# Performance work log

Measured on AMD Instinct MI355X. Metric: run time of the kernel, lower is better.

## Reference

```python
import jax, jax.numpy as jnp
import numpy as np

BS, DX, DY = 64, 512, 512


def setup_inputs() -> dict:
    key = jax.random.key(0)
    k1, k2, k3, k4, k5 = jax.random.split(key, 5)
    # ~1/3 of bins are zero -> ragged nonzero counts per sample
    hist = jax.random.randint(k1, (BS, DX, DY), 0, 3).astype(jnp.float32)
    xlo = jax.random.uniform(k2, (BS,)) * -5.0
    ylo = jax.random.uniform(k3, (BS,)) * -5.0
    x_lims = jnp.stack([xlo, xlo + 1.0 + 9.0 * jax.random.uniform(k4, (BS,))], axis=1)
    y_lims = jnp.stack([ylo, ylo + 1.0 + 9.0 * jax.random.uniform(k5, (BS,))], axis=1)
    return {"hist": hist, "x_lims": x_lims, "y_lims": y_lims}


def _grids(hist, x_lims, y_lims):
    bs, dx, dy = hist.shape
    cxw = (x_lims[:, 1] - x_lims[:, 0]) / dx  # [bs]
    cyw = (y_lims[:, 1] - y_lims[:, 0]) / dy
    cx = (jnp.linspace(0.0, 1.0, dx)[None, :] * cxw[:, None] * (dx - 1)
          + x_lims[:, 0:1] + cxw[:, None] / 2.0)  # [bs, dx]
    cy = (jnp.linspace(0.0, 1.0, dy)[None, :] * cyw[:, None] * (dy - 1)
          + y_lims[:, 0:1] + cyw[:, None] / 2.0)  # [bs, dy]
    hc = jnp.clip(hist, 0.0, 1.0)
    grid_x = cx[:, :, None] * hc  # [bs, dx, dy]
    grid_y = cy[:, None, :] * hc
    return grid_x, grid_y


def reference(hist, x_lims, y_lims):
    # as_sequence=True path. Data-dependent pad_sequence length is not
    # jit-able, so we pad to the full grid length L=dx*dy; the first lens[b]
    # entries per row match torch's ragged output, the rest are zeros
    # (torch's pad value). Stream compaction = stable argsort on the mask.
    bs, dx, dy = hist.shape
    L = dx * dy
    grid_x, grid_y = _grids(hist, x_lims, y_lims)
    mask = (hist != 0).reshape(bs, L)
    order = jnp.argsort(jnp.where(mask, 0, 1).astype(jnp.int32), axis=1, stable=True)
    pc_x = jnp.take_along_axis(grid_x.reshape(bs, L), order, axis=1)
    pc_y = jnp.take_along_axis(grid_y.reshape(bs, L), order, axis=1)
    pc_w = jnp.take_along_axis(hist.reshape(bs, L), order, axis=1)
    pc_w = jnp.where(jnp.take_along_axis(mask, order, axis=1), pc_w, 0.0)
    pc_lens = mask.sum(axis=1).astype(jnp.int32)  # [bs]
    return jnp.stack([pc_x, pc_y], axis=-1), pc_w, pc_lens
```

## Files before the change

kernel.cpp:

```cpp
#include <hip/hip_runtime.h>

#define BS 64
#define DX 512
#define DY 512
#define L (DX * DY)
#define TILE 4096
#define T_PER_S (L / TILE)
#define THREADS 256
#define EPT (TILE / THREADS)

typedef float vfloat2 __attribute__((ext_vector_type(2)));
typedef float vfloat4 __attribute__((ext_vector_type(4)));

__global__ __launch_bounds__(THREADS) void htpc_count(
    const float* __restrict__ hist, int* __restrict__ tile_count) {
  const int tile = blockIdx.x;
  const float4* h4 = (const float4*)(hist + (size_t)tile * TILE);

  int cnt = 0;
#pragma unroll
  for (int r = 0; r < EPT / 4; ++r) {
    float4 v = h4[r * THREADS + threadIdx.x];
    cnt += (v.x != 0.f) + (v.y != 0.f) + (v.z != 0.f) + (v.w != 0.f);
  }
  const int lane = threadIdx.x & 63;
  const int wv = threadIdx.x >> 6;
#pragma unroll
  for (int d = 32; d > 0; d >>= 1) cnt += __shfl_down(cnt, d);
  __shared__ int ws[THREADS / 64];
  if (lane == 0) ws[wv] = cnt;
  __syncthreads();
  if (threadIdx.x == 0)
    tile_count[tile] = ws[0] + ws[1] + ws[2] + ws[3];
}

__global__ __launch_bounds__(THREADS) void htpc_fused(
    const float* __restrict__ hist, const float* __restrict__ x_lims,
    const float* __restrict__ y_lims, const int* __restrict__ tile_count,
    float* __restrict__ out_pc, float* __restrict__ out_w,
    float* __restrict__ out_lens) {
  __shared__ int sidx[TILE];
  __shared__ float sw[TILE];
  __shared__ int s_off[T_PER_S + 1];
  __shared__ int wsum[THREADS / 64];

  const int tile = blockIdx.x;
  const int b = tile >> 6;
  const int t = tile & 63;
  const size_t gbase = (size_t)tile * TILE + (size_t)threadIdx.x * EPT;
  const float4* h4 = (const float4*)(hist + gbase);

  float v[EPT];
#pragma unroll
  for (int i = 0; i < EPT / 4; ++i) {
    float4 a = h4[i];
    v[i * 4 + 0] = a.x;
    v[i * 4 + 1] = a.y;
    v[i * 4 + 2] = a.z;
    v[i * 4 + 3] = a.w;
  }

  if (threadIdx.x < 64) {
    const int c = tile_count[b * T_PER_S + threadIdx.x];
    int incl = c;
#pragma unroll
    for (int d = 1; d < 64; d <<= 1) {
      int n = __shfl_up(incl, d);
      if ((int)threadIdx.x >= d) incl += n;
    }
    s_off[threadIdx.x] = incl - c;
    if (threadIdx.x == 63) {
      s_off[T_PER_S] = incl;
      if (t == 0) out_lens[b] = (float)incl;
    }
  }

  int cnt = 0;
#pragma unroll
  for (int i = 0; i < EPT; ++i) cnt += (v[i] != 0.f);

  const int lane = threadIdx.x & 63;
  const int wv = threadIdx.x >> 6;
  int incl = cnt;
#pragma unroll
  for (int d = 1; d < 64; d <<= 1) {
    int n = __shfl_up(incl, d);
    if (lane >= d) incl += n;
  }
  if (lane == 63) wsum[wv] = incl;
  __syncthreads();
  int wbase = 0, total = 0;
#pragma unroll
  for (int i = 0; i < THREADS / 64; ++i) {
    int s = wsum[i];
    if (i < wv) wbase += s;
    total += s;
  }
  int r = wbase + (incl - cnt);

  const int lidx0 = (int)(gbase - (size_t)b * L);
#pragma unroll
  for (int i = 0; i < EPT; ++i) {
    if (v[i] != 0.f) {
      sidx[r] = lidx0 + i;
      sw[r] = v[i];
      ++r;
    }
  }
  const int off = s_off[t];
  const int len = s_off[T_PER_S];
  __syncthreads();

  const float xlo = x_lims[b * 2], xhi = x_lims[b * 2 + 1];
  const float ylo = y_lims[b * 2], yhi = y_lims[b * 2 + 1];
  const float cxw = (xhi - xlo) / DX;
  const float cyw = (yhi - ylo) / DY;

  vfloat2* pc2 = (vfloat2*)out_pc + (size_t)b * L;
  float* w = out_w + (size_t)b * L;

  if (total > 0) {
    const int ho = off & 1;
    if (ho && threadIdx.x == 0) {
      const int idx = sidx[0];
      vfloat2 p;
      p.x = xlo + cxw * ((float)(idx >> 9) + 0.5f);
      p.y = ylo + cyw * ((float)(idx & 511) + 0.5f);
      pc2[off] = p;
    }
    const int remp = total - ho;
    const int nb = remp >> 1;
    for (int k = threadIdx.x; k < nb; k += THREADS) {
      const int s = ho + 2 * k;
      const int i0 = sidx[s], i1 = sidx[s + 1];
      vfloat4 q;
      q.x = xlo + cxw * ((float)(i0 >> 9) + 0.5f);
      q.y = ylo + cyw * ((float)(i0 & 511) + 0.5f);
      q.z = xlo + cxw * ((float)(i1 >> 9) + 0.5f);
      q.w = ylo + cyw * ((float)(i1 & 511) + 0.5f);
      __builtin_nontemporal_store(q, (vfloat4*)(pc2 + off + s));
    }
    if ((remp & 1) && threadIdx.x == 0) {
      const int s = ho + 2 * nb;
      const int idx = sidx[s];
      vfloat2 p;
      p.x = xlo + cxw * ((float)(idx >> 9) + 0.5f);
      p.y = ylo + cyw * ((float)(idx & 511) + 0.5f);
      pc2[off + s] = p;
    }

    const int hw0 = (4 - (off & 3)) & 3;
    const int hw = hw0 < total ? hw0 : total;
    if ((int)threadIdx.x < hw) w[off + threadIdx.x] = sw[threadIdx.x];
    const int remw = total - hw;
    const int nw = remw >> 2;
    const float* swb = sw + hw;
    float* wb = w + off + hw;
    for (int k = threadIdx.x; k < nw; k += THREADS) {
      vfloat4 q;
      q.x = swb[4 * k + 0];
      q.y = swb[4 * k + 1];
      q.z = swb[4 * k + 2];
      q.w = swb[4 * k + 3];
      __builtin_nontemporal_store(q, (vfloat4*)wb + k);
    }
    const int tw = remw & 3;
    if ((int)threadIdx.x < tw)
      wb[4 * nw + threadIdx.x] = swb[4 * nw + threadIdx.x];
  }

  const int begin = t * TILE;
  const int end = begin + TILE;
  int s0 = (len > begin) ? len : begin;
  if (s0 < end) {
    int a0 = s0;
    if (a0 & 1) {
      if (threadIdx.x == 0) {
        const vfloat2 z2 = {0.f, 0.f};
        __builtin_nontemporal_store(z2, pc2 + a0);
      }
      ++a0;
    }
    {
      vfloat4* p4 = (vfloat4*)(pc2 + a0);
      const int n4 = (end - a0) >> 1;
      const vfloat4 z4 = {0.f, 0.f, 0.f, 0.f};
      for (int k = threadIdx.x; k < n4; k += THREADS)
        __builtin_nontemporal_store(z4, p4 + k);
    }
    const int head = (s0 + 3) & ~3;
    if ((int)threadIdx.x < (head - s0) && (s0 + (int)threadIdx.x) < end)
      __builtin_nontemporal_store(0.f, w + s0 + threadIdx.x);
    if (head < end) {
      vfloat4* w4 = (vfloat4*)(w + head);
      const int n4 = (end - head) >> 2;
      const vfloat4 z4 = {0.f, 0.f, 0.f, 0.f};
      for (int k = threadIdx.x; k < n4; k += THREADS)
        __builtin_nontemporal_store(z4, w4 + k);
    }
  }
}

extern "C" void kernel_launch(void* const* d_in, const int* in_sizes, int n_in,
                              void* d_out, int out_size, void* d_ws,
                              size_t ws_size, hipStream_t stream) {
  const float* hist = (const float*)d_in[0];
  const float* x_lims = (const float*)d_in[1];
  const float* y_lims = (const float*)d_in[2];

  float* out = (float*)d_out;
  float* out_pc = out;
  float* out_w = out + (size_t)BS * L * 2;
  float* out_lens = out_w + (size_t)BS * L;

  int* tile_count = (int*)d_ws;

  htpc_count<<<BS * T_PER_S, THREADS, 0, stream>>>(hist, tile_count);
  htpc_fused<<<BS * T_PER_S, THREADS, 0, stream>>>(
      hist, x_lims, y_lims, tile_count, out_pc, out_w, out_lens);
}
```

Baseline: 257.1 us.

## Shrink compaction tiles to 1024 and fuse tile-offset scan with local scan

Tiles shrink from 4096 to 1024 elements, so each thread handles one float4 and the grid grows to four times as many blocks. The per-sample tile-offset prefix scan, now over 256 tiles, is folded into the intra-block scan by packing the tile count and the local count into one 64-bit value and scanning both together. This aims to raise parallelism and cut per-block register and LDS footprint while removing a separate scan phase. In exchange, every block reads all 256 tile counts of its sample and does 64-bit shuffles, and there are more block launches and partial-alignment edge stores.

```diff
diff --git a/kernel.cpp b/kernel.cpp
--- a/kernel.cpp
+++ b/kernel.cpp
@@ -4,10 +4,11 @@
 #define DX 512
 #define DY 512
 #define L (DX * DY)
-#define TILE 4096
+#define TILE 1024
 #define T_PER_S (L / TILE)
 #define THREADS 256
-#define EPT (TILE / THREADS)
+#define EPT 4
+#define NTILES (BS * T_PER_S)
 
 typedef float vfloat2 __attribute__((ext_vector_type(2)));
 typedef float vfloat4 __attribute__((ext_vector_type(4)));
@@ -15,14 +16,9 @@
 __global__ __launch_bounds__(THREADS) void htpc_count(
     const float* __restrict__ hist, int* __restrict__ tile_count) {
   const int tile = blockIdx.x;
-  const float4* h4 = (const float4*)(hist + (size_t)tile * TILE);
-
-  int cnt = 0;
-#pragma unroll
-  for (int r = 0; r < EPT / 4; ++r) {
-    float4 v = h4[r * THREADS + threadIdx.x];
-    cnt += (v.x != 0.f) + (v.y != 0.f) + (v.z != 0.f) + (v.w != 0.f);
-  }
+  const float4 a = ((const float4*)(hist + (size_t)tile * TILE))[threadIdx.x];
+  int cnt = (a.x != 0.f) + (a.y != 0.f) + (a.z != 0.f) + (a.w != 0.f);
+
   const int lane = threadIdx.x & 63;
   const int wv = threadIdx.x >> 6;
 #pragma unroll
@@ -41,64 +37,49 @@
     float* __restrict__ out_lens) {
   __shared__ int sidx[TILE];
   __shared__ float sw[TILE];
-  __shared__ int s_off[T_PER_S + 1];
-  __shared__ int wsum[THREADS / 64];
-
-  const int tile = blockIdx.x;
-  const int b = tile >> 6;
-  const int t = tile & 63;
-  const size_t gbase = (size_t)tile * TILE + (size_t)threadIdx.x * EPT;
-  const float4* h4 = (const float4*)(hist + gbase);
-
-  float v[EPT];
-#pragma unroll
-  for (int i = 0; i < EPT / 4; ++i) {
-    float4 a = h4[i];
-    v[i * 4 + 0] = a.x;
-    v[i * 4 + 1] = a.y;
-    v[i * 4 + 2] = a.z;
-    v[i * 4 + 3] = a.w;
-  }
-
-  if (threadIdx.x < 64) {
-    const int c = tile_count[b * T_PER_S + threadIdx.x];
-    int incl = c;
-#pragma unroll
-    for (int d = 1; d < 64; d <<= 1) {
-      int n = __shfl_up(incl, d);
-      if ((int)threadIdx.x >= d) incl += n;
-    }
-    s_off[threadIdx.x] = incl - c;
-    if (threadIdx.x == 63) {
-      s_off[T_PER_S] = incl;
-      if (t == 0) out_lens[b] = (float)incl;
-    }
-  }
-
-  int cnt = 0;
-#pragma unroll
-  for (int i = 0; i < EPT; ++i) cnt += (v[i] != 0.f);
-
-  const int lane = threadIdx.x & 63;
-  const int wv = threadIdx.x >> 6;
-  int incl = cnt;
+  __shared__ unsigned long long wsum[THREADS / 64];
+  __shared__ int s_off_mine;
+
+  const int g = blockIdx.x;
+  const int b = g >> 8;
+  const int t = g & 255;
+  const int tid = threadIdx.x;
+
+  const float4 a = ((const float4*)(hist + (size_t)g * TILE))[tid];
+  float v[EPT] = {a.x, a.y, a.z, a.w};
+  int cnt = (v[0] != 0.f) + (v[1] != 0.f) + (v[2] != 0.f) + (v[3] != 0.f);
+
+  const int c_tile = tile_count[b * T_PER_S + tid];
+
+  const int lane = tid & 63;
+  const int wv = tid >> 6;
+  unsigned long long val =
+      ((unsigned long long)(unsigned)c_tile << 32) | (unsigned)cnt;
+  unsigned long long incl = val;
 #pragma unroll
   for (int d = 1; d < 64; d <<= 1) {
-    int n = __shfl_up(incl, d);
+    unsigned long long n = __shfl_up(incl, d);
     if (lane >= d) incl += n;
   }
   if (lane == 63) wsum[wv] = incl;
   __syncthreads();
-  int wbase = 0, total = 0;
+  unsigned long long wbase = 0, total = 0;
 #pragma unroll
   for (int i = 0; i < THREADS / 64; ++i) {
-    int s = wsum[i];
+    unsigned long long s = wsum[i];
     if (i < wv) wbase += s;
     total += s;
   }
-  int r = wbase + (incl - cnt);
-
-  const int lidx0 = (int)(gbase - (size_t)b * L);
+  const unsigned long long ex = wbase + incl - val;
+  int r = (int)(ex & 0xffffffffu);
+  const int offpref = (int)(ex >> 32);
+  const int len = (int)(total >> 32);
+  const int total_cnt = (int)(total & 0xffffffffu);
+
+  if (tid == t) s_off_mine = offpref;
+  if (t == 0 && tid == 0) out_lens[b] = (float)len;
+
+  const int lidx0 = t * TILE + tid * EPT;
 #pragma unroll
   for (int i = 0; i < EPT; ++i) {
     if (v[i] != 0.f) {
@@ -107,9 +88,8 @@
       ++r;
     }
   }
-  const int off = s_off[t];
-  const int len = s_off[T_PER_S];
   __syncthreads();
+  const int off = s_off_mine;
 
   const float xlo = x_lims[b * 2], xhi = x_lims[b * 2 + 1];
   const float ylo = y_lims[b * 2], yhi = y_lims[b * 2 + 1];
@@ -119,18 +99,18 @@
   vfloat2* pc2 = (vfloat2*)out_pc + (size_t)b * L;
   float* w = out_w + (size_t)b * L;
 
-  if (total > 0) {
+  if (total_cnt > 0) {
     const int ho = off & 1;
-    if (ho && threadIdx.x == 0) {
+    if (ho && tid == 0) {
       const int idx = sidx[0];
       vfloat2 p;
       p.x = xlo + cxw * ((float)(idx >> 9) + 0.5f);
       p.y = ylo + cyw * ((float)(idx & 511) + 0.5f);
       pc2[off] = p;
     }
-    const int remp = total - ho;
+    const int remp = total_cnt - ho;
     const int nb = remp >> 1;
-    for (int k = threadIdx.x; k < nb; k += THREADS) {
+    for (int k = tid; k < nb; k += THREADS) {
       const int s = ho + 2 * k;
       const int i0 = sidx[s], i1 = sidx[s + 1];
       vfloat4 q;
@@ -140,7 +120,7 @@
       q.w = ylo + cyw * ((float)(i1 & 511) + 0.5f);
       __builtin_nontemporal_store(q, (vfloat4*)(pc2 + off + s));
     }
-    if ((remp & 1) && threadIdx.x == 0) {
+    if ((remp & 1) && tid == 0) {
       const int s = ho + 2 * nb;
       const int idx = sidx[s];
       vfloat2 p;
@@ -150,13 +130,13 @@
     }
 
     const int hw0 = (4 - (off & 3)) & 3;
-    const int hw = hw0 < total ? hw0 : total;
-    if ((int)threadIdx.x < hw) w[off + threadIdx.x] = sw[threadIdx.x];
-    const int remw = total - hw;
+    const int hw = hw0 < total_cnt ? hw0 : total_cnt;
+    if (tid < hw) w[off + tid] = sw[tid];
+    const int remw = total_cnt - hw;
     const int nw = remw >> 2;
     const float* swb = sw + hw;
     float* wb = w + off + hw;
-    for (int k = threadIdx.x; k < nw; k += THREADS) {
+    for (int k = tid; k < nw; k += THREADS) {
       vfloat4 q;
       q.x = swb[4 * k + 0];
       q.y = swb[4 * k + 1];
@@ -165,8 +145,7 @@
       __builtin_nontemporal_store(q, (vfloat4*)wb + k);
     }
     const int tw = remw & 3;
-    if ((int)threadIdx.x < tw)
-      wb[4 * nw + threadIdx.x] = swb[4 * nw + threadIdx.x];
+    if (tid < tw) wb[4 * nw + tid] = swb[4 * nw + tid];
   }
 
   const int begin = t * TILE;
@@ -175,7 +154,7 @@
   if (s0 < end) {
     int a0 = s0;
     if (a0 & 1) {
-      if (threadIdx.x == 0) {
+      if (tid == 0) {
         const vfloat2 z2 = {0.f, 0.f};
         __builtin_nontemporal_store(z2, pc2 + a0);
       }
@@ -185,17 +164,17 @@
       vfloat4* p4 = (vfloat4*)(pc2 + a0);
       const int n4 = (end - a0) >> 1;
       const vfloat4 z4 = {0.f, 0.f, 0.f, 0.f};
-      for (int k = threadIdx.x; k < n4; k += THREADS)
+      for (int k = tid; k < n4; k += THREADS)
         __builtin_nontemporal_store(z4, p4 + k);
     }
     const int head = (s0 + 3) & ~3;
-    if ((int)threadIdx.x < (head - s0) && (s0 + (int)threadIdx.x) < end)
-      __builtin_nontemporal_store(0.f, w + s0 + threadIdx.x);
+    if (tid < (head - s0) && (s0 + tid) < end)
+      __builtin_nontemporal_store(0.f, w + s0 + tid);
     if (head < end) {
       vfloat4* w4 = (vfloat4*)(w + head);
       const int n4 = (end - head) >> 2;
       const vfloat4 z4 = {0.f, 0.f, 0.f, 0.f};
-      for (int k = threadIdx.x; k < n4; k += THREADS)
+      for (int k = tid; k < n4; k += THREADS)
         __builtin_nontemporal_store(z4, w4 + k);
     }
   }
@@ -215,7 +194,7 @@
 
   int* tile_count = (int*)d_ws;
 
-  htpc_count<<<BS * T_PER_S, THREADS, 0, stream>>>(hist, tile_count);
-  htpc_fused<<<BS * T_PER_S, THREADS, 0, stream>>>(
+  htpc_count<<<NTILES, THREADS, 0, stream>>>(hist, tile_count);
+  htpc_fused<<<NTILES, THREADS, 0, stream>>>(
       hist, x_lims, y_lims, tile_count, out_pc, out_w, out_lens);
 }
```

After: 255.8 us. About the same (-0.5%).
